# Optimization experiments

Hardware: AMD Instinct MI355X
Metric: run time of the kernel (lower is better)

## Reference

```python
import jax, jax.numpy as jnp
import numpy as np

P = 256  # patch_size (init kwarg)


def _unfold3s2(g):
    # g: [B,1,P,P] -> [B,9,L], kernel 3, stride 2, torch Unfold ordering (kh outer, kw inner)
    B = g.shape[0]
    n = (P - 3) // 2 + 1
    cols = [g[:, 0, di:di + 2 * n - 1:2, dj:dj + 2 * n - 1:2]
            for di in range(3) for dj in range(3)]  # each [B,n,n]
    return jnp.stack(cols, axis=1).reshape(B, 9, n * n)


def _fold3s2(patches):
    # patches: [..., 9, L] -> [..., P, P], overlap-add (torch Fold, kernel 3, stride 2)
    lead = patches.shape[:-2]
    n = (P - 3) // 2 + 1
    p = patches.reshape(*lead, 3, 3, n, n)
    out = jnp.zeros((*lead, P, P), patches.dtype)
    for di in range(3):
        for dj in range(3):
            out = out.at[..., di:di + 2 * n - 1:2, dj:dj + 2 * n - 1:2].add(p[..., di, dj, :, :])
    return out


def _maxpool3x3(x):
    # MaxPool2d(3, stride=1, padding=1) on NCHW
    return jax.lax.reduce_window(x, -jnp.inf, jax.lax.max,
                                 (1, 1, 3, 3), (1, 1, 1, 1),
                                 [(0, 0), (0, 0), (1, 1), (1, 1)])


def setup_inputs() -> dict:
    key = jax.random.key(0)
    k1, k2 = jax.random.split(key)
    x = jax.random.uniform(k1, (2, 3, P, P), dtype=jnp.float32)
    ref = jax.random.uniform(k2, (2, 3, P, P), dtype=jnp.float32)
    return {"x": x, "ref": ref, "k": 4}


def reference(x, ref, k):
    B = x.shape[0]
    L = ((P - 3) // 2 + 1) ** 2
    # grayscale proxies
    x_gray = jnp.max(_maxpool3x3(x), axis=1, keepdims=True) - jnp.min(x, axis=1, keepdims=True)
    ref_gray = jnp.mean(ref, axis=1, keepdims=True)
    input_patch = _unfold3s2(x_gray)   # [B,9,L]
    ref_patch = _unfold3s2(ref_gray)   # [B,9,L]
    # faithful to original: mean over patch index (dim 2), norm of UNCENTERED patches over dim 1
    input_norm = (input_patch - jnp.mean(input_patch, axis=2, keepdims=True)) \
        / jnp.linalg.norm(input_patch, axis=1, keepdims=True)
    ref_norm = (ref_patch - jnp.mean(ref_patch, axis=2, keepdims=True)) \
        / jnp.linalg.norm(ref_patch, axis=1, keepdims=True)
    ncc = jnp.einsum('bpl,bpm->blm', input_norm, ref_norm)  # [B,L,L]
    _, idx = jax.lax.top_k(ncc, k)                           # idx: [B,L,k]
    # gather best-matching ref patches for all k at once: [B,k,9,L]
    idx_t = jnp.transpose(idx, (0, 2, 1))                    # [B,k,L]
    ind = jnp.broadcast_to(idx_t[:, :, None, :], (B, k, 9, L))
    src = jnp.broadcast_to(ref_patch[:, None], (B, k, 9, L))
    gathered = jnp.take_along_axis(src, ind, axis=3)         # [B,k,9,L]
    folded = _fold3s2(gathered)                              # [B,k,P,P]
    return jnp.concatenate([x, folded], axis=1)              # [B,3+k,P,P]
```

## Files before the change

### kernel.cpp

```cpp
#include <hip/hip_runtime.h>
#include <math.h>
#include <float.h>

#define PSZ 256
#define NPATCH 127
#define L 16129
#define KTOP 4
#define TMAIN 256
#define RPT 2
#define ROWS_PER_BLOCK (TMAIN * RPT)
#define NROWBLK 32
#define NS 32
#define SEGLEN 512
#define MSTRIDE 512
#define ROWPAD 16384
#define GRP 16
#define APAD 12

static constexpr size_t OFF_REFG = 0;
static constexpr size_t OFF_XG   = OFF_REFG + 2 * PSZ * PSZ;
static constexpr size_t OFF_MUI  = OFF_XG   + 2 * PSZ * PSZ;
static constexpr size_t OFF_MUR  = OFF_MUI  + 20;
static constexpr size_t OFF_A    = OFF_MUR  + 20;
static constexpr size_t OFF_B    = OFF_A    + (size_t)2 * L * APAD;
static constexpr size_t OFF_BT   = OFF_B    + 290324;
static constexpr size_t OFF_IDX  = OFF_BT   + (size_t)2 * L * APAD;
static constexpr size_t OFF_PV   = OFF_IDX  + 2 * L * 4;
static constexpr size_t OFF_PI   = OFF_PV   + (size_t)2 * NS * ROWPAD * 4;

__device__ __forceinline__ void insg(float rm, int gb,
    float& g0, float& g1, float& g2, float& g3,
    int& i0, int& i1, int& i2, int& i3) {
  bool c0 = rm > g0, c1 = rm > g1, c2 = rm > g2, c3 = rm > g3;
  g3 = c2 ? g2 : (c3 ? rm : g3);  i3 = c2 ? i2 : (c3 ? gb : i3);
  g2 = c1 ? g1 : (c2 ? rm : g2);  i2 = c1 ? i1 : (c2 ? gb : i2);
  g1 = c0 ? g0 : (c1 ? rm : g1);  i1 = c0 ? i0 : (c1 ? gb : i1);
  g0 = c0 ? rm : g0;              i0 = c0 ? gb : i0;
}

__device__ __forceinline__ void ins4c(float v, int m,
    float& v0, float& v1, float& v2, float& v3,
    int& x0, int& x1, int& x2, int& x3) {
  bool c0 = (v > v0) || (v == v0 && m < x0);
  bool c1 = (v > v1) || (v == v1 && m < x1);
  bool c2 = (v > v2) || (v == v2 && m < x2);
  bool c3 = (v > v3) || (v == v3 && m < x3);
  v3 = c2 ? v2 : (c3 ? v : v3);  x3 = c2 ? x2 : (c3 ? m : x3);
  v2 = c1 ? v1 : (c2 ? v : v2);  x2 = c1 ? x1 : (c2 ? m : x2);
  v1 = c0 ? v0 : (c1 ? v : v1);  x1 = c0 ? x0 : (c1 ? m : x1);
  v0 = c0 ? v : v0;              x0 = c0 ? m : x0;
}

__global__ void k12_gray(const float* __restrict__ x, const float* __restrict__ ref,
                         float* __restrict__ ws, float* __restrict__ out) {
  __shared__ float sm[34][35];
  int tile = blockIdx.x & 63;
  int b = blockIdx.x >> 6;
  int ty0 = (tile >> 3) << 5, tx0 = (tile & 7) << 5;
  const float* xb = x + (size_t)b * 3 * 65536;
  const float* rb = ref + (size_t)b * 3 * 65536;
  for (int hid = threadIdx.x; hid < 34 * 34; hid += 256) {
    int hy = hid / 34, hx = hid % 34;
    int gy = ty0 + hy - 1, gx = tx0 + hx - 1;
    float m = -FLT_MAX;
    if (gy >= 0 && gy < 256 && gx >= 0 && gx < 256) {
      int pix = gy * 256 + gx;
      m = fmaxf(fmaxf(xb[pix], xb[65536 + pix]), xb[131072 + pix]);
    }
    sm[hy][hx] = m;
  }
  __syncthreads();
  int t4 = threadIdx.x * 4;
  int iy = t4 >> 5, ix = t4 & 31;
  int gy = ty0 + iy, gx = tx0 + ix;
  int pix = gy * 256 + gx;
  float4 c0 = *(const float4*)(xb + pix);
  float4 c1 = *(const float4*)(xb + 65536 + pix);
  float4 c2 = *(const float4*)(xb + 131072 + pix);
  float4 r0 = *(const float4*)(rb + pix);
  float4 r1 = *(const float4*)(rb + 65536 + pix);
  float4 r2 = *(const float4*)(rb + 131072 + pix);
  float cm[7];
#pragma unroll
  for (int c = 0; c < 7; ++c)
    cm[c] = fmaxf(fmaxf(sm[iy][ix + c], sm[iy + 1][ix + c]), sm[iy + 2][ix + c]);
  float cc0[4] = {c0.x, c0.y, c0.z, c0.w};
  float cc1[4] = {c1.x, c1.y, c1.z, c1.w};
  float cc2[4] = {c2.x, c2.y, c2.z, c2.w};
  float rr0[4] = {r0.x, r0.y, r0.z, r0.w};
  float rr1[4] = {r1.x, r1.y, r1.z, r1.w};
  float rr2[4] = {r2.x, r2.y, r2.z, r2.w};
  float xgv[4], rgv[4];
#pragma unroll
  for (int k = 0; k < 4; ++k) {
    float cmin = fminf(fminf(cc0[k], cc1[k]), cc2[k]);
    float mx = fmaxf(fmaxf(cm[k], cm[k + 1]), cm[k + 2]);
    xgv[k] = mx - cmin;
    rgv[k] = (rr0[k] + rr1[k] + rr2[k]) / 3.0f;
  }
  size_t id0 = ((size_t)b << 16) + pix;
  *(float4*)(ws + OFF_XG + id0) = make_float4(xgv[0], xgv[1], xgv[2], xgv[3]);
  *(float4*)(ws + OFF_REFG + id0) = make_float4(rgv[0], rgv[1], rgv[2], rgv[3]);
  float* ob = out + (size_t)b * 7 * 65536 + pix;
  *(float4*)(ob) = c0;
  *(float4*)(ob + 65536) = c1;
  *(float4*)(ob + 131072) = c2;
}

__global__ void k4_mean(float* __restrict__ ws) {
  __shared__ double sm[1024];
  int which = blockIdx.x / 18;
  int bp = blockIdx.x % 18;
  int b = bp / 9, p = bp % 9;
  int di = p / 3, dj = p % 3;
  const float* g = ws + (which ? OFF_REFG : OFF_XG) + ((size_t)b << 16);
  int t = threadIdx.x;
  double s = 0.0;
  int l0 = t * 16;
  if (l0 < L) {
    int l1 = l0 + 16 < L ? l0 + 16 : L;
    int i = l0 / NPATCH, j = l0 % NPATCH;
    for (int l = l0; l < l1; ++l) {
      s += (double)g[(2 * i + di) * PSZ + 2 * j + dj];
      if (++j == NPATCH) { j = 0; ++i; }
    }
  }
  sm[t] = s;
  __syncthreads();
  for (int st = 512; st > 0; st >>= 1) {
    if (t < st) sm[t] += sm[t + st];
    __syncthreads();
  }
  if (t == 0)
    ws[(which ? OFF_MUR : OFF_MUI) + bp] = (float)(sm[0] / (double)L);
}

__global__ void k5_norm(float* __restrict__ ws) {
  int id = blockIdx.x * 256 + threadIdx.x;
  if (id >= 2 * L) return;
  int b = id / L, l = id % L;
  int i = l / NPATCH, j = l % NPATCH;
  const float* xg = ws + OFF_XG + ((size_t)b << 16);
  const float* rg = ws + OFF_REFG + ((size_t)b << 16);
  float vi[9], vr[9];
  float si = 0.f, sr = 0.f;
#pragma unroll
  for (int p = 0; p < 9; ++p) {
    int di = p / 3, dj = p % 3;
    vi[p] = xg[(2 * i + di) * PSZ + 2 * j + dj];
    vr[p] = rg[(2 * i + di) * PSZ + 2 * j + dj];
    si += vi[p] * vi[p];
    sr += vr[p] * vr[p];
  }
  float ni = sqrtf(si), nr = sqrtf(sr);
  float an[12], btn[12];
#pragma unroll
  for (int p = 0; p < 9; ++p) {
    float mi = ws[OFF_MUI + b * 9 + p];
    float mr = ws[OFF_MUR + b * 9 + p];
    float bn = (vr[p] - mr) / nr;
    an[p] = (vi[p] - mi) / ni;
    btn[p] = bn;
    ws[OFF_B + ((size_t)b * 9 + p) * L + l] = bn;
  }
  an[9] = an[10] = an[11] = 0.f;
  btn[9] = btn[10] = btn[11] = 0.f;
  float4* Ap4 = (float4*)(ws + OFF_A + (size_t)(b * L + l) * APAD);
  Ap4[0] = make_float4(an[0], an[1], an[2], an[3]);
  Ap4[1] = make_float4(an[4], an[5], an[6], an[7]);
  Ap4[2] = make_float4(an[8], an[9], an[10], an[11]);
  float4* Bt4 = (float4*)(ws + OFF_BT + (size_t)(b * L + l) * APAD);
  Bt4[0] = make_float4(btn[0], btn[1], btn[2], btn[3]);
  Bt4[1] = make_float4(btn[4], btn[5], btn[6], btn[7]);
  Bt4[2] = make_float4(btn[8], btn[9], btn[10], btn[11]);
}

__global__ __launch_bounds__(TMAIN, 2) void k6_topk(float* __restrict__ ws) {
  __shared__ float lds[9 * MSTRIDE];

  int bid = blockIdx.x;
  int seg = bid & (NS - 1);
  int rowblk = (bid >> 5) & (NROWBLK - 1);
  int b = bid >> 10;
  int m0 = seg << 9;
  int mend = m0 + SEGLEN;
  if (mend > L) mend = L;
  int mlen = mend - m0;

  const float* Bg = ws + OFF_B + (size_t)b * 9 * L + m0;
  for (int p = 0; p < 9; ++p)
    for (int mm = threadIdx.x; mm < mlen; mm += TMAIN)
      lds[p * MSTRIDE + mm] = Bg[(size_t)p * L + mm];
  __syncthreads();

  int row0 = rowblk * ROWS_PER_BLOCK + threadIdx.x * RPT;
  int r0 = row0 < L - 1 ? row0 : L - 1;
  int r1 = row0 + 1 < L - 1 ? row0 + 1 : L - 1;
  float a0[9], a1[9];
  {
    const float4* Ap0 = (const float4*)(ws + OFF_A + ((size_t)b * L + r0) * APAD);
    const float4* Ap1 = (const float4*)(ws + OFF_A + ((size_t)b * L + r1) * APAD);
    float4 u0 = Ap0[0], u1 = Ap0[1], u2 = Ap0[2];
    float4 w0 = Ap1[0], w1 = Ap1[1], w2 = Ap1[2];
    a0[0] = u0.x; a0[1] = u0.y; a0[2] = u0.z; a0[3] = u0.w;
    a0[4] = u1.x; a0[5] = u1.y; a0[6] = u1.z; a0[7] = u1.w; a0[8] = u2.x;
    a1[0] = w0.x; a1[1] = w0.y; a1[2] = w0.z; a1[3] = w0.w;
    a1[4] = w1.x; a1[5] = w1.y; a1[6] = w1.z; a1[7] = w1.w; a1[8] = w2.x;
  }

  float g00 = -FLT_MAX, g01 = g00, g02 = g00, g03 = g00;
  float g10 = g00, g11 = g00, g12 = g00, g13 = g00;
  int i00 = 0, i01 = 0, i02 = 0, i03 = 0;
  int i10 = 0, i11 = 0, i12 = 0, i13 = 0;

  int nfull = mlen >> 4;
  for (int g = 0; g < nfull; ++g) {
    int mm = g << 4;
    float rm0 = -FLT_MAX, rm1 = -FLT_MAX;
#pragma unroll
    for (int q = 0; q < 4; ++q) {
      float s00, s01, s02, s03, s10, s11, s12, s13;
#pragma unroll
      for (int p = 0; p < 9; ++p) {
        const float4 bq = *reinterpret_cast<const float4*>(&lds[p * MSTRIDE + mm + q * 4]);
        if (p == 0) {
          s00 = a0[0] * bq.x; s01 = a0[0] * bq.y; s02 = a0[0] * bq.z; s03 = a0[0] * bq.w;
          s10 = a1[0] * bq.x; s11 = a1[0] * bq.y; s12 = a1[0] * bq.z; s13 = a1[0] * bq.w;
        } else {
          s00 = fmaf(a0[p], bq.x, s00); s01 = fmaf(a0[p], bq.y, s01);
          s02 = fmaf(a0[p], bq.z, s02); s03 = fmaf(a0[p], bq.w, s03);
          s10 = fmaf(a1[p], bq.x, s10); s11 = fmaf(a1[p], bq.y, s11);
          s12 = fmaf(a1[p], bq.z, s12); s13 = fmaf(a1[p], bq.w, s13);
        }
      }
      rm0 = fmaxf(rm0, fmaxf(fmaxf(s00, s01), fmaxf(s02, s03)));
      rm1 = fmaxf(rm1, fmaxf(fmaxf(s10, s11), fmaxf(s12, s13)));
    }
    int gb = m0 + mm;
    insg(rm0, gb, g00, g01, g02, g03, i00, i01, i02, i03);
    insg(rm1, gb, g10, g11, g12, g13, i10, i11, i12, i13);
  }
  int tb = nfull << 4;
  if (tb < mlen) {
    float rt0 = -FLT_MAX, rt1 = -FLT_MAX;
    for (int mm = tb; mm < mlen; ++mm) {
      float bb = lds[mm];
      float sv0 = a0[0] * bb, sv1 = a1[0] * bb;
#pragma unroll
      for (int p = 1; p < 9; ++p) {
        bb = lds[p * MSTRIDE + mm];
        sv0 = fmaf(a0[p], bb, sv0); sv1 = fmaf(a1[p], bb, sv1);
      }
      rt0 = fmaxf(rt0, sv0); rt1 = fmaxf(rt1, sv1);
    }
    insg(rt0, m0 + tb, g00, g01, g02, g03, i00, i01, i02, i03);
    insg(rt1, m0 + tb, g10, g11, g12, g13, i10, i11, i12, i13);
  }

  int* wsi = (int*)ws;
  if (row0 < L) {
    size_t base = (((size_t)b * NS + seg) * ROWPAD + row0) * 4;
    ws[OFF_PV + base + 0] = g00; ws[OFF_PV + base + 1] = g01;
    ws[OFF_PV + base + 2] = g02; ws[OFF_PV + base + 3] = g03;
    wsi[OFF_PI + base + 0] = i00; wsi[OFF_PI + base + 1] = i01;
    wsi[OFF_PI + base + 2] = i02; wsi[OFF_PI + base + 3] = i03;
  }
  if (row0 + 1 < L) {
    size_t base = (((size_t)b * NS + seg) * ROWPAD + row0 + 1) * 4;
    ws[OFF_PV + base + 0] = g10; ws[OFF_PV + base + 1] = g11;
    ws[OFF_PV + base + 2] = g12; ws[OFF_PV + base + 3] = g13;
    wsi[OFF_PI + base + 0] = i10; wsi[OFF_PI + base + 1] = i11;
    wsi[OFF_PI + base + 2] = i12; wsi[OFF_PI + base + 3] = i13;
  }
}

__global__ void k7_merge(float* __restrict__ ws) {
  int id = blockIdx.x * 256 + threadIdx.x;
  if (id >= 2 * L) return;
  int b = id / L, row = id % L;
  const int* wsi_c = (const int*)ws;

  float v0 = -FLT_MAX, v1 = v0, v2 = v0, v3 = v0;
  int x0 = 0x7FFFFFFF, x1 = x0, x2 = x0, x3 = x0;
  for (int s = 0; s < NS; ++s) {
    size_t base = (((size_t)b * NS + s) * ROWPAD + row) * 4;
#pragma unroll
    for (int q = 0; q < 4; ++q) {
      float val = ws[OFF_PV + base + q];
      int gb = wsi_c[OFF_PI + base + q];
      ins4c(val, gb, v0, v1, v2, v3, x0, x1, x2, x3);
    }
  }

  float a[9];
  {
    const float4* Ap4 = (const float4*)(ws + OFF_A + ((size_t)b * L + row) * APAD);
    float4 u0 = Ap4[0], u1 = Ap4[1], u2 = Ap4[2];
    a[0] = u0.x; a[1] = u0.y; a[2] = u0.z; a[3] = u0.w;
    a[4] = u1.x; a[5] = u1.y; a[6] = u1.z; a[7] = u1.w; a[8] = u2.x;
  }

  int gbs[4] = {x0, x1, x2, x3};
  float w0 = -FLT_MAX, w1 = w0, w2 = w0, w3 = w0;
  int y0 = 0x7FFFFFFF, y1 = y0, y2 = y0, y3 = y0;
#pragma unroll
  for (int slot = 0; slot < 4; ++slot) {
    int gb = gbs[slot];
    int se = ((gb >> 9) + 1) << 9;
    int ge = gb + GRP;
    if (ge > se) ge = se;
    if (ge > L) ge = L;
    for (int mm = gb; mm < ge; ++mm) {
      const float4* bt4 = (const float4*)(ws + OFF_BT + ((size_t)b * L + mm) * APAD);
      float4 b0 = bt4[0], b1 = bt4[1], b2 = bt4[2];
      float s = a[0] * b0.x;
      s = fmaf(a[1], b0.y, s); s = fmaf(a[2], b0.z, s); s = fmaf(a[3], b0.w, s);
      s = fmaf(a[4], b1.x, s); s = fmaf(a[5], b1.y, s); s = fmaf(a[6], b1.z, s);
      s = fmaf(a[7], b1.w, s); s = fmaf(a[8], b2.x, s);
      ins4c(s, mm, w0, w1, w2, w3, y0, y1, y2, y3);
    }
  }
  int* wsi = (int*)ws;
  size_t ib = OFF_IDX + (size_t)id * 4;
  wsi[ib] = y0; wsi[ib + 1] = y1; wsi[ib + 2] = y2; wsi[ib + 3] = y3;
}

__global__ void k8_fold(const float* __restrict__ ws, float* __restrict__ out) {
  int id = blockIdx.x * 256 + threadIdx.x;
  if (id >= 2 * PSZ * PSZ) return;
  int b = id >> 16;
  int pix = id & 0xFFFF;
  int y = pix >> 8, xx = pix & 255;
  const int* wsi = (const int*)ws;
  const float* rg = ws + OFF_REFG + ((size_t)b << 16);
  float acc0 = 0.f, acc1 = 0.f, acc2 = 0.f, acc3 = 0.f;
  for (int di = 0; di < 3; ++di) {
    int yy = y - di;
    if (yy < 0 || (yy & 1) || (yy >> 1) >= NPATCH) continue;
    int i = yy >> 1;
    for (int dj = 0; dj < 3; ++dj) {
      int xc = xx - dj;
      if (xc < 0 || (xc & 1) || (xc >> 1) >= NPATCH) continue;
      int j = xc >> 1;
      int l = i * NPATCH + j;
      const int4 m4 = *(const int4*)(wsi + OFF_IDX + ((size_t)b * L + l) * 4);
      acc0 += rg[(2 * (m4.x / NPATCH) + di) * PSZ + 2 * (m4.x % NPATCH) + dj];
      acc1 += rg[(2 * (m4.y / NPATCH) + di) * PSZ + 2 * (m4.y % NPATCH) + dj];
      acc2 += rg[(2 * (m4.z / NPATCH) + di) * PSZ + 2 * (m4.z % NPATCH) + dj];
      acc3 += rg[(2 * (m4.w / NPATCH) + di) * PSZ + 2 * (m4.w % NPATCH) + dj];
    }
  }
  float* ob = out + ((size_t)b * 7 + 3) * 65536 + pix;
  ob[0] = acc0;
  ob[65536] = acc1;
  ob[2 * 65536] = acc2;
  ob[3 * 65536] = acc3;
}

extern "C" void kernel_launch(void* const* d_in, const int* in_sizes, int n_in,
                              void* d_out, int out_size, void* d_ws, size_t ws_size,
                              hipStream_t stream) {
  const float* x = (const float*)d_in[0];
  const float* ref = (const float*)d_in[1];
  float* ws = (float*)d_ws;
  float* out = (float*)d_out;

  k12_gray<<<128, 256, 0, stream>>>(x, ref, ws, out);
  k4_mean<<<36, 1024, 0, stream>>>(ws);
  k5_norm<<<(2 * L + 255) / 256, 256, 0, stream>>>(ws);
  k6_topk<<<2 * NROWBLK * NS, TMAIN, 0, stream>>>(ws);
  k7_merge<<<(2 * L + 255) / 256, 256, 0, stream>>>(ws);
  k8_fold<<<(2 * PSZ * PSZ + 255) / 256, 256, 0, stream>>>(ws, out);
}
```

Before: 228.3 us.

## Fuse pipeline into single cooperative persistent kernel with grid syncs

```diff
diff --git a/kernel.cpp b/kernel.cpp
--- a/kernel.cpp
+++ b/kernel.cpp
@@ -1,10 +1,14 @@
 #include <hip/hip_runtime.h>
+#include <hip/hip_cooperative_groups.h>
 #include <math.h>
 #include <float.h>
+
+namespace cg = cooperative_groups;
 
 #define PSZ 256
 #define NPATCH 127
 #define L 16129
+#define LPAD 16132
 #define KTOP 4
 #define TMAIN 256
 #define RPT 2
@@ -16,17 +20,18 @@
 #define ROWPAD 16384
 #define GRP 16
 #define APAD 12
+#define GRID_MAIN 2048
+#define NCHUNK 56
 
 static constexpr size_t OFF_REFG = 0;
 static constexpr size_t OFF_XG   = OFF_REFG + 2 * PSZ * PSZ;
-static constexpr size_t OFF_MUI  = OFF_XG   + 2 * PSZ * PSZ;
-static constexpr size_t OFF_MUR  = OFF_MUI  + 20;
-static constexpr size_t OFF_A    = OFF_MUR  + 20;
-static constexpr size_t OFF_B    = OFF_A    + (size_t)2 * L * APAD;
-static constexpr size_t OFF_BT   = OFF_B    + 290324;
-static constexpr size_t OFF_IDX  = OFF_BT   + (size_t)2 * L * APAD;
-static constexpr size_t OFF_PV   = OFF_IDX  + 2 * L * 4;
-static constexpr size_t OFF_PI   = OFF_PV   + (size_t)2 * NS * ROWPAD * 4;
+static constexpr size_t OFF_A    = OFF_XG + 2 * PSZ * PSZ + 40;
+static constexpr size_t OFF_B    = OFF_A + (size_t)2 * L * APAD;
+static constexpr size_t OFF_BT   = OFF_B + (size_t)2 * 9 * LPAD;
+static constexpr size_t OFF_IDX  = OFF_BT + (size_t)2 * L * APAD;
+static constexpr size_t OFF_PV   = OFF_IDX + 2 * L * 4;
+static constexpr size_t OFF_PI   = OFF_PV + (size_t)2 * NS * ROWPAD * 4;
+static constexpr size_t OFF_PAR  = OFF_PV;
 
 __device__ __forceinline__ void insg(float rm, int gb,
     float& g0, float& g1, float& g2, float& g3,
@@ -51,134 +56,114 @@
   v0 = c0 ? v : v0;              x0 = c0 ? m : x0;
 }
 
-__global__ void k12_gray(const float* __restrict__ x, const float* __restrict__ ref,
-                         float* __restrict__ ws, float* __restrict__ out) {
-  __shared__ float sm[34][35];
-  int tile = blockIdx.x & 63;
-  int b = blockIdx.x >> 6;
-  int ty0 = (tile >> 3) << 5, tx0 = (tile & 7) << 5;
-  const float* xb = x + (size_t)b * 3 * 65536;
-  const float* rb = ref + (size_t)b * 3 * 65536;
-  for (int hid = threadIdx.x; hid < 34 * 34; hid += 256) {
-    int hy = hid / 34, hx = hid % 34;
-    int gy = ty0 + hy - 1, gx = tx0 + hx - 1;
+
+__device__ void phase1_gray(int gid, const float* __restrict__ x,
+                            const float* __restrict__ ref,
+                            float* __restrict__ ws, float* __restrict__ out) {
+  if (gid < 2 * PSZ * PSZ) {
+    int b = gid >> 16, pix = gid & 0xFFFF;
+    int y = pix >> 8, xx = pix & 255;
+    const float* xb = x + (size_t)b * 3 * 65536;
+    const float* rb = ref + (size_t)b * 3 * 65536;
+    float c0 = xb[pix], c1 = xb[65536 + pix], c2 = xb[131072 + pix];
+    float cmin = fminf(fminf(c0, c1), c2);
     float m = -FLT_MAX;
-    if (gy >= 0 && gy < 256 && gx >= 0 && gx < 256) {
-      int pix = gy * 256 + gx;
-      m = fmaxf(fmaxf(xb[pix], xb[65536 + pix]), xb[131072 + pix]);
-    }
-    sm[hy][hx] = m;
-  }
-  __syncthreads();
-  int t4 = threadIdx.x * 4;
-  int iy = t4 >> 5, ix = t4 & 31;
-  int gy = ty0 + iy, gx = tx0 + ix;
-  int pix = gy * 256 + gx;
-  float4 c0 = *(const float4*)(xb + pix);
-  float4 c1 = *(const float4*)(xb + 65536 + pix);
-  float4 c2 = *(const float4*)(xb + 131072 + pix);
-  float4 r0 = *(const float4*)(rb + pix);
-  float4 r1 = *(const float4*)(rb + 65536 + pix);
-  float4 r2 = *(const float4*)(rb + 131072 + pix);
-  float cm[7];
-#pragma unroll
-  for (int c = 0; c < 7; ++c)
-    cm[c] = fmaxf(fmaxf(sm[iy][ix + c], sm[iy + 1][ix + c]), sm[iy + 2][ix + c]);
-  float cc0[4] = {c0.x, c0.y, c0.z, c0.w};
-  float cc1[4] = {c1.x, c1.y, c1.z, c1.w};
-  float cc2[4] = {c2.x, c2.y, c2.z, c2.w};
-  float rr0[4] = {r0.x, r0.y, r0.z, r0.w};
-  float rr1[4] = {r1.x, r1.y, r1.z, r1.w};
-  float rr2[4] = {r2.x, r2.y, r2.z, r2.w};
-  float xgv[4], rgv[4];
-#pragma unroll
-  for (int k = 0; k < 4; ++k) {
-    float cmin = fminf(fminf(cc0[k], cc1[k]), cc2[k]);
-    float mx = fmaxf(fmaxf(cm[k], cm[k + 1]), cm[k + 2]);
-    xgv[k] = mx - cmin;
-    rgv[k] = (rr0[k] + rr1[k] + rr2[k]) / 3.0f;
-  }
-  size_t id0 = ((size_t)b << 16) + pix;
-  *(float4*)(ws + OFF_XG + id0) = make_float4(xgv[0], xgv[1], xgv[2], xgv[3]);
-  *(float4*)(ws + OFF_REFG + id0) = make_float4(rgv[0], rgv[1], rgv[2], rgv[3]);
-  float* ob = out + (size_t)b * 7 * 65536 + pix;
-  *(float4*)(ob) = c0;
-  *(float4*)(ob + 65536) = c1;
-  *(float4*)(ob + 131072) = c2;
-}
-
-__global__ void k4_mean(float* __restrict__ ws) {
-  __shared__ double sm[1024];
-  int which = blockIdx.x / 18;
-  int bp = blockIdx.x % 18;
-  int b = bp / 9, p = bp % 9;
-  int di = p / 3, dj = p % 3;
-  const float* g = ws + (which ? OFF_REFG : OFF_XG) + ((size_t)b << 16);
-  int t = threadIdx.x;
-  double s = 0.0;
-  int l0 = t * 16;
-  if (l0 < L) {
-    int l1 = l0 + 16 < L ? l0 + 16 : L;
-    int i = l0 / NPATCH, j = l0 % NPATCH;
-    for (int l = l0; l < l1; ++l) {
+#pragma unroll
+    for (int dy = -1; dy <= 1; ++dy) {
+      int yy = y + dy;
+      if (yy < 0 || yy > 255) continue;
+#pragma unroll
+      for (int dx = -1; dx <= 1; ++dx) {
+        int xc = xx + dx;
+        if (xc < 0 || xc > 255) continue;
+        int pp = yy * 256 + xc;
+        m = fmaxf(m, fmaxf(fmaxf(xb[pp], xb[65536 + pp]), xb[131072 + pp]));
+      }
+    }
+    size_t id0 = ((size_t)b << 16) + pix;
+    ws[OFF_XG + id0] = m - cmin;
+    ws[OFF_REFG + id0] = (rb[pix] + rb[65536 + pix] + rb[131072 + pix]) / 3.0f;
+    float* ob = out + (size_t)b * 7 * 65536 + pix;
+    ob[0] = c0; ob[65536] = c1; ob[131072] = c2;
+  }
+}
+
+__device__ void phase2_partial(int bid, int tid, float* lds, float* __restrict__ ws) {
+  if (bid < 36 * NCHUNK) {
+    int cmb = bid / NCHUNK, chunk = bid % NCHUNK;
+    int which = cmb / 18, rest = cmb % 18;
+    int b = rest / 9, p = rest % 9;
+    int di = p / 3, dj = p % 3;
+    const float* g = ws + (which ? OFF_REFG : OFF_XG) + ((size_t)b << 16);
+    int l0 = chunk * 288;
+    int lend = (chunk == NCHUNK - 1) ? L : l0 + 288;
+    double s = 0.0;
+    for (int l = l0 + tid; l < lend; l += TMAIN) {
+      int i = l / NPATCH, j = l % NPATCH;
       s += (double)g[(2 * i + di) * PSZ + 2 * j + dj];
-      if (++j == NPATCH) { j = 0; ++i; }
-    }
-  }
-  sm[t] = s;
-  __syncthreads();
-  for (int st = 512; st > 0; st >>= 1) {
-    if (t < st) sm[t] += sm[t + st];
+    }
+    double* smd = (double*)lds;
+    smd[tid] = s;
     __syncthreads();
-  }
-  if (t == 0)
-    ws[(which ? OFF_MUR : OFF_MUI) + bp] = (float)(sm[0] / (double)L);
-}
-
-__global__ void k5_norm(float* __restrict__ ws) {
-  int id = blockIdx.x * 256 + threadIdx.x;
-  if (id >= 2 * L) return;
-  int b = id / L, l = id % L;
-  int i = l / NPATCH, j = l % NPATCH;
-  const float* xg = ws + OFF_XG + ((size_t)b << 16);
-  const float* rg = ws + OFF_REFG + ((size_t)b << 16);
-  float vi[9], vr[9];
-  float si = 0.f, sr = 0.f;
-#pragma unroll
-  for (int p = 0; p < 9; ++p) {
-    int di = p / 3, dj = p % 3;
-    vi[p] = xg[(2 * i + di) * PSZ + 2 * j + dj];
-    vr[p] = rg[(2 * i + di) * PSZ + 2 * j + dj];
-    si += vi[p] * vi[p];
-    sr += vr[p] * vr[p];
-  }
-  float ni = sqrtf(si), nr = sqrtf(sr);
-  float an[12], btn[12];
-#pragma unroll
-  for (int p = 0; p < 9; ++p) {
-    float mi = ws[OFF_MUI + b * 9 + p];
-    float mr = ws[OFF_MUR + b * 9 + p];
-    float bn = (vr[p] - mr) / nr;
-    an[p] = (vi[p] - mi) / ni;
-    btn[p] = bn;
-    ws[OFF_B + ((size_t)b * 9 + p) * L + l] = bn;
-  }
-  an[9] = an[10] = an[11] = 0.f;
-  btn[9] = btn[10] = btn[11] = 0.f;
-  float4* Ap4 = (float4*)(ws + OFF_A + (size_t)(b * L + l) * APAD);
-  Ap4[0] = make_float4(an[0], an[1], an[2], an[3]);
-  Ap4[1] = make_float4(an[4], an[5], an[6], an[7]);
-  Ap4[2] = make_float4(an[8], an[9], an[10], an[11]);
-  float4* Bt4 = (float4*)(ws + OFF_BT + (size_t)(b * L + l) * APAD);
-  Bt4[0] = make_float4(btn[0], btn[1], btn[2], btn[3]);
-  Bt4[1] = make_float4(btn[4], btn[5], btn[6], btn[7]);
-  Bt4[2] = make_float4(btn[8], btn[9], btn[10], btn[11]);
-}
-
-__global__ __launch_bounds__(TMAIN, 2) void k6_topk(float* __restrict__ ws) {
-  __shared__ float lds[9 * MSTRIDE];
-
-  int bid = blockIdx.x;
+    for (int st = 128; st > 0; st >>= 1) {
+      if (tid < st) smd[tid] += smd[tid + st];
+      __syncthreads();
+    }
+    if (tid == 0) ((double*)(ws + OFF_PAR))[cmb * NCHUNK + chunk] = smd[0];
+  }
+}
+
+__device__ void phase3_norm(int bid, int tid, float* lds, float* __restrict__ ws) {
+  if (bid < 127) {
+    if (tid < 36) {
+      const double* par = (const double*)(ws + OFF_PAR);
+      double s = 0.0;
+      for (int c = 0; c < NCHUNK; ++c) s += par[tid * NCHUNK + c];
+      lds[tid] = (float)(s / (double)L);
+    }
+    __syncthreads();
+    int gid = bid * TMAIN + tid;
+    if (gid < 2 * L) {
+      int b = gid / L, l = gid % L;
+      int i = l / NPATCH, j = l % NPATCH;
+      const float* xg = ws + OFF_XG + ((size_t)b << 16);
+      const float* rg = ws + OFF_REFG + ((size_t)b << 16);
+      float vi[9], vr[9];
+      float si = 0.f, sr = 0.f;
+#pragma unroll
+      for (int p = 0; p < 9; ++p) {
+        int di = p / 3, dj = p % 3;
+        vi[p] = xg[(2 * i + di) * PSZ + 2 * j + dj];
+        vr[p] = rg[(2 * i + di) * PSZ + 2 * j + dj];
+        si += vi[p] * vi[p];
+        sr += vr[p] * vr[p];
+      }
+      float ni = sqrtf(si), nr = sqrtf(sr);
+      float an[12], btn[12];
+#pragma unroll
+      for (int p = 0; p < 9; ++p) {
+        float mi = lds[b * 9 + p];
+        float mr = lds[18 + b * 9 + p];
+        float bn = (vr[p] - mr) / nr;
+        an[p] = (vi[p] - mi) / ni;
+        btn[p] = bn;
+        ws[OFF_B + ((size_t)b * 9 + p) * LPAD + l] = bn;
+      }
+      an[9] = an[10] = an[11] = 0.f;
+      btn[9] = btn[10] = btn[11] = 0.f;
+      float4* Ap4 = (float4*)(ws + OFF_A + (size_t)(b * L + l) * APAD);
+      Ap4[0] = make_float4(an[0], an[1], an[2], an[3]);
+      Ap4[1] = make_float4(an[4], an[5], an[6], an[7]);
+      Ap4[2] = make_float4(an[8], an[9], an[10], an[11]);
+      float4* Bt4 = (float4*)(ws + OFF_BT + (size_t)(b * L + l) * APAD);
+      Bt4[0] = make_float4(btn[0], btn[1], btn[2], btn[3]);
+      Bt4[1] = make_float4(btn[4], btn[5], btn[6], btn[7]);
+      Bt4[2] = make_float4(btn[8], btn[9], btn[10], btn[11]);
+    }
+  }
+}
+
+__device__ void phase4_topk(int bid, int tid, float* lds, float* __restrict__ ws) {
   int seg = bid & (NS - 1);
   int rowblk = (bid >> 5) & (NROWBLK - 1);
   int b = bid >> 10;
@@ -187,13 +172,18 @@
   if (mend > L) mend = L;
   int mlen = mend - m0;
 
-  const float* Bg = ws + OFF_B + (size_t)b * 9 * L + m0;
-  for (int p = 0; p < 9; ++p)
-    for (int mm = threadIdx.x; mm < mlen; mm += TMAIN)
-      lds[p * MSTRIDE + mm] = Bg[(size_t)p * L + mm];
+  const float* Bg = ws + OFF_B + (size_t)b * 9 * LPAD + m0;
+  int nf4 = mlen >> 2;
+  for (int p = 0; p < 9; ++p) {
+    const float4* src = (const float4*)(Bg + (size_t)p * LPAD);
+    float4* dst = (float4*)(lds + p * MSTRIDE);
+    for (int idx = tid; idx < nf4; idx += TMAIN) dst[idx] = src[idx];
+    for (int mm = (nf4 << 2) + tid; mm < mlen; mm += TMAIN)
+      lds[p * MSTRIDE + mm] = Bg[(size_t)p * LPAD + mm];
+  }
   __syncthreads();
 
-  int row0 = rowblk * ROWS_PER_BLOCK + threadIdx.x * RPT;
+  int row0 = rowblk * ROWS_PER_BLOCK + tid * RPT;
   int r0 = row0 < L - 1 ? row0 : L - 1;
   int r1 = row0 + 1 < L - 1 ? row0 + 1 : L - 1;
   float a0[9], a1[9];
@@ -274,87 +264,126 @@
   }
 }
 
-__global__ void k7_merge(float* __restrict__ ws) {
-  int id = blockIdx.x * 256 + threadIdx.x;
-  if (id >= 2 * L) return;
-  int b = id / L, row = id % L;
-  const int* wsi_c = (const int*)ws;
-
-  float v0 = -FLT_MAX, v1 = v0, v2 = v0, v3 = v0;
-  int x0 = 0x7FFFFFFF, x1 = x0, x2 = x0, x3 = x0;
-  for (int s = 0; s < NS; ++s) {
-    size_t base = (((size_t)b * NS + s) * ROWPAD + row) * 4;
-#pragma unroll
-    for (int q = 0; q < 4; ++q) {
-      float val = ws[OFF_PV + base + q];
-      int gb = wsi_c[OFF_PI + base + q];
-      ins4c(val, gb, v0, v1, v2, v3, x0, x1, x2, x3);
-    }
-  }
-
-  float a[9];
-  {
-    const float4* Ap4 = (const float4*)(ws + OFF_A + ((size_t)b * L + row) * APAD);
-    float4 u0 = Ap4[0], u1 = Ap4[1], u2 = Ap4[2];
-    a[0] = u0.x; a[1] = u0.y; a[2] = u0.z; a[3] = u0.w;
-    a[4] = u1.x; a[5] = u1.y; a[6] = u1.z; a[7] = u1.w; a[8] = u2.x;
-  }
-
-  int gbs[4] = {x0, x1, x2, x3};
-  float w0 = -FLT_MAX, w1 = w0, w2 = w0, w3 = w0;
-  int y0 = 0x7FFFFFFF, y1 = y0, y2 = y0, y3 = y0;
-#pragma unroll
-  for (int slot = 0; slot < 4; ++slot) {
-    int gb = gbs[slot];
-    int se = ((gb >> 9) + 1) << 9;
-    int ge = gb + GRP;
-    if (ge > se) ge = se;
-    if (ge > L) ge = L;
-    for (int mm = gb; mm < ge; ++mm) {
-      const float4* bt4 = (const float4*)(ws + OFF_BT + ((size_t)b * L + mm) * APAD);
-      float4 b0 = bt4[0], b1 = bt4[1], b2 = bt4[2];
-      float s = a[0] * b0.x;
-      s = fmaf(a[1], b0.y, s); s = fmaf(a[2], b0.z, s); s = fmaf(a[3], b0.w, s);
-      s = fmaf(a[4], b1.x, s); s = fmaf(a[5], b1.y, s); s = fmaf(a[6], b1.z, s);
-      s = fmaf(a[7], b1.w, s); s = fmaf(a[8], b2.x, s);
-      ins4c(s, mm, w0, w1, w2, w3, y0, y1, y2, y3);
-    }
-  }
-  int* wsi = (int*)ws;
-  size_t ib = OFF_IDX + (size_t)id * 4;
-  wsi[ib] = y0; wsi[ib + 1] = y1; wsi[ib + 2] = y2; wsi[ib + 3] = y3;
-}
-
-__global__ void k8_fold(const float* __restrict__ ws, float* __restrict__ out) {
-  int id = blockIdx.x * 256 + threadIdx.x;
-  if (id >= 2 * PSZ * PSZ) return;
-  int b = id >> 16;
-  int pix = id & 0xFFFF;
-  int y = pix >> 8, xx = pix & 255;
-  const int* wsi = (const int*)ws;
-  const float* rg = ws + OFF_REFG + ((size_t)b << 16);
-  float acc0 = 0.f, acc1 = 0.f, acc2 = 0.f, acc3 = 0.f;
-  for (int di = 0; di < 3; ++di) {
-    int yy = y - di;
-    if (yy < 0 || (yy & 1) || (yy >> 1) >= NPATCH) continue;
-    int i = yy >> 1;
-    for (int dj = 0; dj < 3; ++dj) {
-      int xc = xx - dj;
-      if (xc < 0 || (xc & 1) || (xc >> 1) >= NPATCH) continue;
-      int j = xc >> 1;
-      int l = i * NPATCH + j;
-      const int4 m4 = *(const int4*)(wsi + OFF_IDX + ((size_t)b * L + l) * 4);
-      acc0 += rg[(2 * (m4.x / NPATCH) + di) * PSZ + 2 * (m4.x % NPATCH) + dj];
-      acc1 += rg[(2 * (m4.y / NPATCH) + di) * PSZ + 2 * (m4.y % NPATCH) + dj];
-      acc2 += rg[(2 * (m4.z / NPATCH) + di) * PSZ + 2 * (m4.z % NPATCH) + dj];
-      acc3 += rg[(2 * (m4.w / NPATCH) + di) * PSZ + 2 * (m4.w % NPATCH) + dj];
-    }
-  }
-  float* ob = out + ((size_t)b * 7 + 3) * 65536 + pix;
-  ob[0] = acc0;
-  ob[65536] = acc1;
-  ob[2 * 65536] = acc2;
-  ob[3 * 65536] = acc3;
+__device__ void phase5_merge(int gid, float* __restrict__ ws) {
+  if (gid < 2 * L) {
+    int b = gid / L, row = gid % L;
+    const int* wsi_c = (const int*)ws;
+    float v0 = -FLT_MAX, v1 = v0, v2 = v0, v3 = v0;
+    int x0 = 0x7FFFFFFF, x1 = x0, x2 = x0, x3 = x0;
+    for (int s = 0; s < NS; ++s) {
+      size_t base = (((size_t)b * NS + s) * ROWPAD + row) * 4;
+#pragma unroll
+      for (int q = 0; q < 4; ++q) {
+        float val = ws[OFF_PV + base + q];
+        int gb = wsi_c[OFF_PI + base + q];
+        ins4c(val, gb, v0, v1, v2, v3, x0, x1, x2, x3);
+      }
+    }
+    float a[9];
+    {
+      const float4* Ap4 = (const float4*)(ws + OFF_A + ((size_t)b * L + row) * APAD);
+      float4 u0 = Ap4[0], u1 = Ap4[1], u2 = Ap4[2];
+      a[0] = u0.x; a[1] = u0.y; a[2] = u0.z; a[3] = u0.w;
+      a[4] = u1.x; a[5] = u1.y; a[6] = u1.z; a[7] = u1.w; a[8] = u2.x;
+    }
+    int gbs[4] = {x0, x1, x2, x3};
+    float w0 = -FLT_MAX, w1 = w0, w2 = w0, w3 = w0;
+    int y0 = 0x7FFFFFFF, y1 = y0, y2 = y0, y3 = y0;
+#pragma unroll
+    for (int slot = 0; slot < 4; ++slot) {
+      int gb = gbs[slot];
+      int se = ((gb >> 9) + 1) << 9;
+      int ge = gb + GRP;
+      if (ge > se) ge = se;
+      if (ge > L) ge = L;
+      for (int mm = gb; mm < ge; ++mm) {
+        const float4* bt4 = (const float4*)(ws + OFF_BT + ((size_t)b * L + mm) * APAD);
+        float4 b0 = bt4[0], b1 = bt4[1], b2 = bt4[2];
+        float s = a[0] * b0.x;
+        s = fmaf(a[1], b0.y, s); s = fmaf(a[2], b0.z, s); s = fmaf(a[3], b0.w, s);
+        s = fmaf(a[4], b1.x, s); s = fmaf(a[5], b1.y, s); s = fmaf(a[6], b1.z, s);
+        s = fmaf(a[7], b1.w, s); s = fmaf(a[8], b2.x, s);
+        ins4c(s, mm, w0, w1, w2, w3, y0, y1, y2, y3);
+      }
+    }
+    int* wsi = (int*)ws;
+    size_t ib = OFF_IDX + (size_t)gid * 4;
+    wsi[ib] = y0; wsi[ib + 1] = y1; wsi[ib + 2] = y2; wsi[ib + 3] = y3;
+  }
+}
+
+__device__ void phase6_fold(int gid, const float* __restrict__ ws, float* __restrict__ out) {
+  if (gid < 2 * PSZ * PSZ) {
+    int b = gid >> 16, pix = gid & 0xFFFF;
+    int y = pix >> 8, xx = pix & 255;
+    const int* wsi = (const int*)ws;
+    const float* rg = ws + OFF_REFG + ((size_t)b << 16);
+    float acc0 = 0.f, acc1 = 0.f, acc2 = 0.f, acc3 = 0.f;
+    for (int di = 0; di < 3; ++di) {
+      int yy = y - di;
+      if (yy < 0 || (yy & 1) || (yy >> 1) >= NPATCH) continue;
+      int i = yy >> 1;
+      for (int dj = 0; dj < 3; ++dj) {
+        int xc = xx - dj;
+        if (xc < 0 || (xc & 1) || (xc >> 1) >= NPATCH) continue;
+        int j = xc >> 1;
+        int l = i * NPATCH + j;
+        const int4 m4 = *(const int4*)(wsi + OFF_IDX + ((size_t)b * L + l) * 4);
+        acc0 += rg[(2 * (m4.x / NPATCH) + di) * PSZ + 2 * (m4.x % NPATCH) + dj];
+        acc1 += rg[(2 * (m4.y / NPATCH) + di) * PSZ + 2 * (m4.y % NPATCH) + dj];
+        acc2 += rg[(2 * (m4.z / NPATCH) + di) * PSZ + 2 * (m4.z % NPATCH) + dj];
+        acc3 += rg[(2 * (m4.w / NPATCH) + di) * PSZ + 2 * (m4.w % NPATCH) + dj];
+      }
+    }
+    float* ob = out + ((size_t)b * 7 + 3) * 65536 + pix;
+    ob[0] = acc0;
+    ob[65536] = acc1;
+    ob[2 * 65536] = acc2;
+    ob[3 * 65536] = acc3;
+  }
+}
+
+__global__ __launch_bounds__(TMAIN, 2) void mega(const float* __restrict__ x,
+    const float* __restrict__ ref, float* __restrict__ ws, float* __restrict__ out) {
+  cg::grid_group gg = cg::this_grid();
+  __shared__ __align__(16) float lds[9 * MSTRIDE];
+  const int bid = blockIdx.x, tid = threadIdx.x;
+  const int gid = bid * TMAIN + tid;
+
+  phase1_gray(gid, x, ref, ws, out);
+  gg.sync();
+  phase2_partial(bid, tid, lds, ws);
+  gg.sync();
+  phase3_norm(bid, tid, lds, ws);
+  gg.sync();
+  phase4_topk(bid, tid, lds, ws);
+  gg.sync();
+  phase5_merge(gid, ws);
+  gg.sync();
+  phase6_fold(gid, ws, out);
+}
+
+__global__ void kA_gray(const float* __restrict__ x, const float* __restrict__ ref,
+                        float* __restrict__ ws, float* __restrict__ out) {
+  phase1_gray(blockIdx.x * TMAIN + threadIdx.x, x, ref, ws, out);
+}
+__global__ void kB_par(float* __restrict__ ws) {
+  __shared__ __align__(16) float lds[TMAIN * 2];
+  phase2_partial(blockIdx.x, threadIdx.x, lds, ws);
+}
+__global__ void kC_norm(float* __restrict__ ws) {
+  __shared__ __align__(16) float lds[64];
+  phase3_norm(blockIdx.x, threadIdx.x, lds, ws);
+}
+__global__ __launch_bounds__(TMAIN, 2) void kD_topk(float* __restrict__ ws) {
+  __shared__ __align__(16) float lds[9 * MSTRIDE];
+  phase4_topk(blockIdx.x, threadIdx.x, lds, ws);
+}
+__global__ void kE_merge(float* __restrict__ ws) {
+  phase5_merge(blockIdx.x * TMAIN + threadIdx.x, ws);
+}
+__global__ void kF_fold(const float* __restrict__ ws, float* __restrict__ out) {
+  phase6_fold(blockIdx.x * TMAIN + threadIdx.x, ws, out);
 }
 
 extern "C" void kernel_launch(void* const* d_in, const int* in_sizes, int n_in,
@@ -365,10 +394,24 @@
   float* ws = (float*)d_ws;
   float* out = (float*)d_out;
 
-  k12_gray<<<128, 256, 0, stream>>>(x, ref, ws, out);
-  k4_mean<<<36, 1024, 0, stream>>>(ws);
-  k5_norm<<<(2 * L + 255) / 256, 256, 0, stream>>>(ws);
-  k6_topk<<<2 * NROWBLK * NS, TMAIN, 0, stream>>>(ws);
-  k7_merge<<<(2 * L + 255) / 256, 256, 0, stream>>>(ws);
-  k8_fold<<<(2 * PSZ * PSZ + 255) / 256, 256, 0, stream>>>(ws, out);
-}
+  int dev = 0;
+  hipGetDevice(&dev);
+  int coop = 0, ncu = 0, occ = 0;
+  hipDeviceGetAttribute(&coop, hipDeviceAttributeCooperativeLaunch, dev);
+  hipDeviceGetAttribute(&ncu, hipDeviceAttributeMultiprocessorCount, dev);
+  hipOccupancyMaxActiveBlocksPerMultiprocessor(&occ, (const void*)mega, TMAIN, 0);
+  bool use_coop = coop != 0 && (long)occ * (long)ncu >= GRID_MAIN;
+
+  if (use_coop) {
+    void* args[] = {(void*)&x, (void*)&ref, (void*)&ws, (void*)&out};
+    hipLaunchCooperativeKernel((const void*)mega, dim3(GRID_MAIN), dim3(TMAIN),
+                               args, 0, stream);
+  } else {
+    kA_gray<<<512, TMAIN, 0, stream>>>(x, ref, ws, out);
+    kB_par<<<36 * NCHUNK, TMAIN, 0, stream>>>(ws);
+    kC_norm<<<127, TMAIN, 0, stream>>>(ws);
+    kD_topk<<<GRID_MAIN, TMAIN, 0, stream>>>(ws);
+    kE_merge<<<127, TMAIN, 0, stream>>>(ws);
+    kF_fold<<<512, TMAIN, 0, stream>>>(ws, out);
+  }
+}
```

Measured after the change: 265.7 us. 1.16x slower.
